# Kernel optimization log

Hardware: AMD Instinct MI355X
Metric: run time of the kernel (lower is better)

The kernel has to match this reference:

```python
import jax, jax.numpy as jnp
import numpy as np

B, D, W = 2048, 512, 512
DEPTH = 6
N_BINS = 2 ** DEPTH          # 64 leaves
N_NODES = 2 ** DEPTH - 1     # 63 inner nodes


def build_indices(depth: int) -> np.ndarray:
    """Root-to-leaf path index table into hstack([probs, 1-probs]).
    Index j selects probs[:, j]; index j + N selects 1 - probs[:, j]."""
    n = 2 ** depth - 1
    paths = []
    for b in range(2 ** depth):
        node, path = 0, []
        for level in range(depth):
            bit = (b >> (depth - 1 - level)) & 1
            path.append(node if bit == 0 else node + n)
            node = 2 * node + 1 + bit
        paths.append(path)
    return np.asarray(paths, dtype=np.int32)  # [2**depth, depth]


def setup_inputs() -> dict:
    key = jax.random.key(0)
    k1, k2, k3, k4 = jax.random.split(key, 4)
    x = jax.random.normal(k1, (B, D), dtype=jnp.float32)
    ray = jax.random.normal(k2, (1, D), dtype=jnp.float32)  # kaiming-normal init
    w_i = jnp.zeros((1, N_NODES), dtype=jnp.float32)
    b_i = jax.random.normal(k3, (1, N_NODES), dtype=jnp.float32)
    a_i = 5.0 * jnp.ones((1, N_NODES), dtype=jnp.float32)
    # kaiming-normal over fan_in = input_width
    inner_transforms = jax.random.normal(k4, (N_BINS, D, W), dtype=jnp.float32) * np.float32((2.0 / D) ** 0.5)
    idx = jnp.asarray(build_indices(DEPTH))  # [64, 6] int32
    return {"x": x, "ray": ray, "w_i": w_i, "b_i": b_i, "a_i": a_i,
            "inner_transforms": inner_transforms, "idx": idx}


def reference(x, ray, w_i, b_i, a_i, inner_transforms, idx):
    eps = 1e-8
    # angles: arccos(cosine_similarity(x, ray)) / pi  -> [B]
    xn = jnp.maximum(jnp.linalg.norm(x, axis=1), eps)
    rn = jnp.maximum(jnp.linalg.norm(ray, axis=1), eps)  # [1]
    cos = (x @ ray[0]) / (xn * rn)
    angles = jnp.arccos(cos) / jnp.pi  # [B]
    # per-node decision probabilities: [B, N_NODES]
    node_fns = (0.5 + jax.nn.sigmoid(w_i)) * angles[:, None] - jax.nn.sigmoid(b_i)
    decisions = jax.nn.sigmoid(node_fns * (1.0 + a_i))
    # tree-indexed gather + product over path -> soft bin distribution [B, N_BINS]
    stacked = jnp.concatenate([decisions, 1.0 - decisions], axis=1)  # [B, 2N]
    bins, depth = idx.shape
    gathered = stacked[:, idx.reshape(-1)].reshape(x.shape[0], bins, depth)
    distribution = jnp.prod(gathered, axis=2)  # [B, L]
    # per-bin linear transforms, weighted by the distribution
    inner = jnp.einsum('bi,liw->blw', x, inner_transforms)  # [B, L, W]
    return jnp.einsum('bl,blo->bo', distribution, inner)  # [B, W]
```

## Files before the change

### kernel.cpp

```cpp
#include <hip/hip_runtime.h>
#include <math.h>

typedef float  f32x4  __attribute__((ext_vector_type(4)));
typedef float  f32x2  __attribute__((ext_vector_type(2)));
typedef short  bf16x8 __attribute__((ext_vector_type(8)));
typedef unsigned short u16x8 __attribute__((ext_vector_type(8)));
typedef unsigned short u16x4 __attribute__((ext_vector_type(4)));

#define B_ROWS 2048
#define D_DIM  512
#define W_DIM  512
#define N_NODES 63
#define N_BINS  64
#define K_TOT   32768
#define DEPS    1e-12f

#define STR2(x) #x
#define WAITVM(n) asm volatile("s_waitcnt vmcnt(" STR2(n) ")" ::: "memory")

__device__ __forceinline__ unsigned short f2bf(float f) {
    union { float f; unsigned int u; } v; v.f = f;
    unsigned int u = v.u;
    return (unsigned short)((u + 0x7fffu + ((u >> 16) & 1u)) >> 16);
}

__device__ __forceinline__ float sigmoidf_(float z) {
    return 1.0f / (1.0f + expf(-z));
}

__device__ __forceinline__ void load_lds16(const void* g, void* l) {
    __builtin_amdgcn_global_load_lds(
        (const __attribute__((address_space(1))) unsigned int*)g,
        (__attribute__((address_space(3))) unsigned int*)l,
        16, 0, 0);
}

__global__ __launch_bounds__(256) void k_pre(
    const float* __restrict__ x, const float* __restrict__ ray,
    const float* __restrict__ w_i, const float* __restrict__ b_i,
    const float* __restrict__ a_i, const int* __restrict__ idx,
    const float* __restrict__ T,
    float* __restrict__ dist, unsigned short* __restrict__ xb,
    unsigned short* __restrict__ Tt)
{
    __shared__ float tile[64][65];
    const int bid = blockIdx.x;
    const int t   = threadIdx.x;

    if (bid < 4096) {
        const int i0 = (bid & 7) * 64;
        const int w0 = ((bid >> 3) & 7) * 64;
        const int l  = bid >> 6;

        const int w4 = (t & 15) * 4;
        const int ir = t >> 4;
        const float* src = T + ((size_t)(l * 512 + i0)) * 512 + w0;
#pragma unroll
        for (int p = 0; p < 4; ++p) {
            int i = ir + p * 16;
            f32x4 v = *(const f32x4*)(src + (size_t)i * 512 + w4);
            tile[i][w4 + 0] = v.x; tile[i][w4 + 1] = v.y;
            tile[i][w4 + 2] = v.z; tile[i][w4 + 3] = v.w;
        }
        __syncthreads();
#pragma unroll
        for (int rep = 0; rep < 2; ++rep) {
            int id = t + rep * 256;
            int w  = id >> 3;
            int c  = id & 7;
            u16x8 o;
#pragma unroll
            for (int j = 0; j < 8; ++j) o[j] = f2bf(tile[c * 8 + j][w]);
            *(u16x8*)(Tt + (size_t)(w0 + w) * K_TOT + l * 512 + i0 + c * 8) = o;
        }
        return;
    }

    const int pb   = bid - 4096;
    const int wid  = t >> 6;
    const int lane = t & 63;
    const int row  = pb * 4 + wid;
    const float* xr = x + (size_t)row * D_DIM;

    float dotv = 0.f, xx = 0.f, rr = 0.f;
#pragma unroll
    for (int j = 0; j < 2; ++j) {
        f32x4 xv = *(const f32x4*)(xr  + j * 256 + lane * 4);
        f32x4 rv = *(const f32x4*)(ray + j * 256 + lane * 4);
        dotv += xv.x * rv.x + xv.y * rv.y + xv.z * rv.z + xv.w * rv.w;
        xx   += xv.x * xv.x + xv.y * xv.y + xv.z * xv.z + xv.w * xv.w;
        rr   += rv.x * rv.x + rv.y * rv.y + rv.z * rv.z + rv.w * rv.w;
        u16x4 o;
        o[0] = f2bf(xv.x); o[1] = f2bf(xv.y); o[2] = f2bf(xv.z); o[3] = f2bf(xv.w);
        *(u16x4*)(xb + (size_t)row * D_DIM + j * 256 + lane * 4) = o;
    }
#pragma unroll
    for (int off = 1; off < 64; off <<= 1) {
        dotv += __shfl_xor(dotv, off, 64);
        xx   += __shfl_xor(xx,   off, 64);
        rr   += __shfl_xor(rr,   off, 64);
    }
    float xn = fmaxf(sqrtf(xx), 1e-8f);
    float rn = fmaxf(sqrtf(rr), 1e-8f);
    float cosv = dotv / (xn * rn);
    cosv = fminf(1.f, fmaxf(-1.f, cosv));
    float angle = acosf(cosv) * 0.31830988618379067f;

    float dec = 0.f;
    if (lane < N_NODES) {
        float sw = sigmoidf_(w_i[lane]);
        float sb = sigmoidf_(b_i[lane]);
        float nf = (0.5f + sw) * angle - sb;
        dec = sigmoidf_(nf * (1.0f + a_i[lane]));
    }

    float p = 1.f;
#pragma unroll
    for (int v = 0; v < 6; ++v) {
        int j = idx[lane * 6 + v];
        int node = (j < N_NODES) ? j : j - N_NODES;
        float d = __shfl(dec, node, 64);
        p *= (j < N_NODES) ? d : (1.0f - d);
    }
    dist[(size_t)row * N_BINS + lane] = p;
}

__global__ __launch_bounds__(512, 2) void k_gemm16(
    const unsigned short* __restrict__ xb, const unsigned short* __restrict__ Tt,
    const float* __restrict__ dist, float* __restrict__ part)
{
    __shared__ unsigned short As[2][256 * 64];
    __shared__ unsigned short Bs[2][256 * 64];
    __shared__ float distS[256 * 4];

    const int b    = blockIdx.x;
    const int xcd  = b & 7;
    const int g    = b >> 3;
    const int z    = xcd * 2 + (g & 1);
    const int tile = g >> 1;
    const int bm0  = (tile & 7) * 256;
    const int bn0  = (tile >> 3) * 256;
    const int l0   = z * 4;

    const int t    = threadIdx.x;
    const int lane = t & 63;
    const int wid  = t >> 6;
    const int wm   = wid >> 2;
    const int wn   = wid & 3;
    const int lq = lane >> 4, lr = lane & 15;

    const int srow = t >> 3;
    const int c    = t & 7;

    f32x4 acc[8][4];
#pragma unroll
    for (int a = 0; a < 8; ++a)
#pragma unroll
        for (int bb = 0; bb < 4; ++bb)
            acc[a][bb] = (f32x4){0.f, 0.f, 0.f, 0.f};

#define SGA(u_, slot_, g_)                                                    \
    {                                                                         \
        const int i0_  = ((u_) & 7) * 64;                                     \
        const int row_ = srow + (g_) * 64;                                    \
        const int cg_  = c ^ (row_ & 7);                                      \
        load_lds16(xb + (size_t)(bm0 + row_) * D_DIM + i0_ + cg_ * 8,         \
                   &As[slot_][row_ * 64 + c * 8]);                            \
    }
#define SGB(u_, slot_, g_)                                                    \
    {                                                                         \
        const int l_   = l0 + ((u_) >> 3);                                    \
        const int i0_  = ((u_) & 7) * 64;                                     \
        const int row_ = srow + (g_) * 64;                                    \
        const int cg_  = c ^ (row_ & 7);                                      \
        load_lds16(Tt + (size_t)(bn0 + row_) * K_TOT + (size_t)l_ * 512       \
                       + i0_ + cg_ * 8,                                       \
                   &Bs[slot_][row_ * 64 + c * 8]);                            \
    }

#define RD_A(dst, fmb)                                                        \
    _Pragma("unroll") for (int f = 0; f < 4; ++f)                             \
    _Pragma("unroll") for (int ks = 0; ks < 2; ++ks) {                        \
        int row = ((fmb) + f) * 32 + wm * 16 + lr;                            \
        dst[f][ks] = *(const bf16x8*)&As[rs][row * 64 +                       \
                       (((ks * 4 + lq) ^ (row & 7)) * 8)];                    \
    }
#define RD_B(dst, fnb)                                                        \
    _Pragma("unroll") for (int f = 0; f < 2; ++f)                             \
    _Pragma("unroll") for (int ks = 0; ks < 2; ++ks) {                        \
        int row = ((fnb) + f) * 64 + wn * 16 + lr;                            \
        dst[f][ks] = *(const bf16x8*)&Bs[rs][row * 64 +                       \
                       (((ks * 4 + lq) ^ (row & 7)) * 8)];                    \
    }
#define MM(fmb, afv, bfv, fnb)                                                \
    __builtin_amdgcn_s_setprio(1);                                            \
    _Pragma("unroll") for (int f = 0; f < 4; ++f)                             \
    _Pragma("unroll") for (int e = 0; e < 2; ++e)                             \
    _Pragma("unroll") for (int ks = 0; ks < 2; ++ks)                          \
        acc[(fmb) + f][(fnb) + e] = __builtin_amdgcn_mfma_f32_16x16x32_bf16(  \
            afv[f][ks], bfv[e][ks], acc[(fmb) + f][(fnb) + e], 0, 0, 0);      \
    __builtin_amdgcn_s_setprio(0);

#define LGKM0                                                                 \
    asm volatile("s_waitcnt lgkmcnt(0)" ::: "memory");                        \
    __builtin_amdgcn_sched_barrier(0);

#define TILE(u_, V0_, V1_, PF_)                                               \
  {                                                                           \
    const int rs = (u_) & 1, ss = rs ^ 1;                                     \
                                                       \
    RD_A(afr, 0) RD_B(bfr0, 0)                                                \
    if (PF_) { SGA((u_) + 1, ss, 0) SGA((u_) + 1, ss, 1) }                    \
    __builtin_amdgcn_s_barrier();                                             \
    LGKM0                                                                     \
    MM(0, afr, bfr0, 0)                                                       \
    WAITVM(V0_);                                                              \
    __builtin_amdgcn_s_barrier();                                             \
                                                       \
    RD_B(bfr1, 2)                                                             \
    if (PF_) { SGB((u_) + 1, ss, 0) SGB((u_) + 1, ss, 1) }                    \
    __builtin_amdgcn_s_barrier();                                             \
    LGKM0                                                                     \
    MM(0, afr, bfr1, 2)                                                       \
    WAITVM(V1_);                                                              \
    __builtin_amdgcn_s_barrier();                                             \
                                                       \
    RD_A(afr, 4)                                                              \
    if (PF_) { SGB((u_) + 1, ss, 2) SGB((u_) + 1, ss, 3) }                    \
    __builtin_amdgcn_s_barrier();                                             \
    LGKM0                                                                     \
    MM(4, afr, bfr0, 0)                                                       \
    __builtin_amdgcn_s_barrier();                                             \
                                                       \
    if (PF_) { SGA((u_) + 1, ss, 2) SGA((u_) + 1, ss, 3) }                    \
    __builtin_amdgcn_s_barrier();                                             \
    __builtin_amdgcn_sched_barrier(0);                                        \
    MM(4, afr, bfr1, 2)                                                       \
    WAITVM(4);                                                                \
    __builtin_amdgcn_s_barrier();                                             \
  }

    bf16x8 afr[4][2], bfr0[2][2], bfr1[2][2];

    if (t < 256)
        load_lds16(dist + (size_t)(bm0 + t) * N_BINS + l0, &distS[t * 4]);
    SGA(0, 0, 0) SGA(0, 0, 1)
    SGB(0, 0, 0) SGB(0, 0, 1)
    SGB(0, 0, 2) SGB(0, 0, 3)
    SGA(0, 0, 2) SGA(0, 0, 3)
    WAITVM(4);
    __builtin_amdgcn_s_barrier();

    for (int u = 0; u < 31; ++u) {
        if ((u & 7) == 0 && u > 0) {
            const int li = (u >> 3) - 1;
#pragma unroll
            for (int fm = 0; fm < 8; ++fm)
#pragma unroll
                for (int r = 0; r < 4; ++r) {
                    int ml = fm * 32 + wm * 16 + lq * 4 + r;
                    float dp = fmaxf(distS[ml * 4 + li],     DEPS);
                    float dn = fmaxf(distS[ml * 4 + li + 1], DEPS);
                    float ratio = dp * __builtin_amdgcn_rcpf(dn);
#pragma unroll
                    for (int fn = 0; fn < 4; ++fn)
                        acc[fm][fn][r] *= ratio;
                }
        }
        TILE(u, 4, 4, true)
    }
    TILE(31, 2, 0, false)

#undef TILE
#undef LGKM0
#undef MM
#undef RD_A
#undef RD_B
#undef SGA
#undef SGB

    float* Cp = part + (size_t)z * (B_ROWS * W_DIM);
#pragma unroll
    for (int fm = 0; fm < 8; ++fm)
#pragma unroll
        for (int r = 0; r < 4; ++r) {
            int ml = fm * 32 + wm * 16 + lq * 4 + r;
            float dv = fmaxf(distS[ml * 4 + 3], DEPS);
            int m = bm0 + ml;
#pragma unroll
            for (int fn = 0; fn < 4; ++fn) {
                int col = bn0 + fn * 64 + wn * 16 + lr;
                Cp[(size_t)m * W_DIM + col] = acc[fm][fn][r] * dv;
            }
        }
}

__global__ __launch_bounds__(512, 2) void k_gemm10(
    const unsigned short* __restrict__ xb, const unsigned short* __restrict__ Tt,
    const float* __restrict__ dist, float* __restrict__ part)
{
    __shared__ unsigned short As[3][256 * 64];
    __shared__ unsigned short Bs[3][128 * 64];

    const int b    = blockIdx.x;
    const int z    = b & 7;
    const int tile = b >> 3;
    const int bm0  = (tile & 7) * 256;
    const int bn0  = (tile >> 3) * 128;
    const int l0   = z * 8;

    const int t    = threadIdx.x;
    const int lane = t & 63;
    const int wid  = t >> 6;
    const int wm = wid >> 1, wn = wid & 1;
    const int lq = lane >> 4, lr = lane & 15;

    const int srow = t >> 3;
    const int c    = t & 7;

    f32x4 acc[4][4];
#pragma unroll
    for (int a = 0; a < 4; ++a)
#pragma unroll
        for (int bb = 0; bb < 4; ++bb)
            acc[a][bb] = (f32x4){0.f, 0.f, 0.f, 0.f};

#define STAGE_A(u_, slot_, g_)                                                \
    {                                                                         \
        const int i0_  = ((u_) & 7) * 64;                                     \
        const int row_ = srow + (g_) * 64;                                    \
        const int cg_  = c ^ (row_ & 7);                                      \
        load_lds16(xb + (size_t)(bm0 + row_) * D_DIM + i0_ + cg_ * 8,         \
                   &As[slot_][row_ * 64 + c * 8]);                            \
    }
#define STAGE_B(u_, slot_, g_)                                                \
    {                                                                         \
        const int l_   = l0 + ((u_) >> 3);                                    \
        const int i0_  = ((u_) & 7) * 64;                                     \
        const int row_ = srow + (g_) * 64;                                    \
        const int cg_  = c ^ (row_ & 7);                                      \
        load_lds16(Tt + (size_t)(bn0 + row_) * K_TOT + (size_t)l_ * 512       \
                       + i0_ + cg_ * 8,                                       \
                   &Bs[slot_][row_ * 64 + c * 8]);                            \
    }

    STAGE_A(0, 0, 0) STAGE_A(0, 0, 1) STAGE_A(0, 0, 2) STAGE_A(0, 0, 3)
    STAGE_B(0, 0, 0) STAGE_B(0, 0, 1)
    STAGE_A(1, 1, 0) STAGE_A(1, 1, 1) STAGE_A(1, 1, 2) STAGE_A(1, 1, 3)
    STAGE_B(1, 1, 0) STAGE_B(1, 1, 1)

    int rs = 0;
    for (int u = 0; u < 64; ++u) {
        if (u < 63) WAITVM(6);
        else        WAITVM(0);
        __builtin_amdgcn_s_barrier();

        if ((u & 7) == 0 && u > 0) {
            const int l = l0 + (u >> 3);
#pragma unroll
            for (int fm = 0; fm < 4; ++fm)
#pragma unroll
                for (int r = 0; r < 4; ++r) {
                    int m = bm0 + wm * 64 + fm * 16 + lq * 4 + r;
                    f32x2 dd = *(const f32x2*)(dist + (size_t)m * N_BINS + (l - 1));
                    float dp = fmaxf(dd.x, DEPS);
                    float dn = fmaxf(dd.y, DEPS);
                    float ratio = dp * __builtin_amdgcn_rcpf(dn);
#pragma unroll
                    for (int fn = 0; fn < 4; ++fn)
                        acc[fm][fn][r] *= ratio;
                }
        }

        const int ws_ = (rs == 0) ? 2 : rs - 1;
        const bool pf = (u + 2 < 64);

        {
            bf16x8 af[4], bfv[4];
#pragma unroll
            for (int fm = 0; fm < 4; ++fm) {
                int m = wm * 64 + fm * 16 + lr;
                af[fm] = *(const bf16x8*)&As[rs][m * 64 + ((lq ^ (m & 7)) * 8)];
            }
#pragma unroll
            for (int fn = 0; fn < 4; ++fn) {
                int n = wn * 64 + fn * 16 + lr;
                bfv[fn] = *(const bf16x8*)&Bs[rs][n * 64 + ((lq ^ (n & 7)) * 8)];
            }
            if (pf) { STAGE_A(u + 2, ws_, 0) STAGE_A(u + 2, ws_, 1) STAGE_A(u + 2, ws_, 2) }
            __builtin_amdgcn_s_setprio(1);
#pragma unroll
            for (int fm = 0; fm < 4; ++fm)
#pragma unroll
                for (int fn = 0; fn < 4; ++fn)
                    acc[fm][fn] = __builtin_amdgcn_mfma_f32_16x16x32_bf16(
                        af[fm], bfv[fn], acc[fm][fn], 0, 0, 0);
            __builtin_amdgcn_s_setprio(0);
        }
        __builtin_amdgcn_s_barrier();
        {
            bf16x8 af[4], bfv[4];
#pragma unroll
            for (int fm = 0; fm < 4; ++fm) {
                int m = wm * 64 + fm * 16 + lr;
                af[fm] = *(const bf16x8*)&As[rs][m * 64 + (((4 + lq) ^ (m & 7)) * 8)];
            }
#pragma unroll
            for (int fn = 0; fn < 4; ++fn) {
                int n = wn * 64 + fn * 16 + lr;
                bfv[fn] = *(const bf16x8*)&Bs[rs][n * 64 + (((4 + lq) ^ (n & 7)) * 8)];
            }
            if (pf) { STAGE_A(u + 2, ws_, 3) STAGE_B(u + 2, ws_, 0) STAGE_B(u + 2, ws_, 1) }
            __builtin_amdgcn_s_setprio(1);
#pragma unroll
            for (int fm = 0; fm < 4; ++fm)
#pragma unroll
                for (int fn = 0; fn < 4; ++fn)
                    acc[fm][fn] = __builtin_amdgcn_mfma_f32_16x16x32_bf16(
                        af[fm], bfv[fn], acc[fm][fn], 0, 0, 0);
            __builtin_amdgcn_s_setprio(0);
        }

        rs = (rs == 2) ? 0 : rs + 1;
    }
#undef STAGE_A
#undef STAGE_B

    float* Cp = part + (size_t)z * (B_ROWS * W_DIM);
#pragma unroll
    for (int fm = 0; fm < 4; ++fm)
#pragma unroll
        for (int r = 0; r < 4; ++r) {
            int m = bm0 + wm * 64 + fm * 16 + lq * 4 + r;
            float dl = fmaxf(dist[(size_t)m * N_BINS + (l0 + 7)], DEPS);
#pragma unroll
            for (int fn = 0; fn < 4; ++fn) {
                int col = bn0 + wn * 64 + fn * 16 + lr;
                Cp[(size_t)m * W_DIM + col] = acc[fm][fn][r] * dl;
            }
        }
}

__global__ __launch_bounds__(256) void k_reduce(
    const float* __restrict__ part, float* __restrict__ out, int nsplit)
{
    int i = (blockIdx.x * 256 + threadIdx.x) * 4;
    f32x4 s = *(const f32x4*)(part + i);
    for (int p = 1; p < nsplit; ++p)
        s += *(const f32x4*)(part + (size_t)p * (B_ROWS * W_DIM) + i);
    *(f32x4*)(out + i) = s;
}

__global__ __launch_bounds__(256, 2) void k_gemm_bt(
    const float* __restrict__ x, const float* __restrict__ dist,
    const unsigned short* __restrict__ Tt, float* __restrict__ part,
    int kchunk)
{
    __shared__ unsigned short As[128][72];
    __shared__ unsigned short Bs[128][64];

    const int bm0 = blockIdx.x * 128;
    const int bn0 = blockIdx.y * 128;
    const int kbase = blockIdx.z * kchunk;

    const int lane = threadIdx.x & 63;
    const int wid  = threadIdx.x >> 6;
    const int wm = wid >> 1, wn = wid & 1;
    const int lq = lane >> 4, lr = lane & 15;

    f32x4 acc[4][4];
#pragma unroll
    for (int a = 0; a < 4; ++a)
#pragma unroll
        for (int b = 0; b < 4; ++b)
            acc[a][b] = (f32x4){0.f, 0.f, 0.f, 0.f};

    const int iters = kchunk / 64;
    for (int it = 0; it < iters; ++it) {
        const int k0 = kbase + it * 64;
        const int l  = k0 >> 9;
        const int i0 = k0 & 511;
#pragma unroll
        for (int r2 = 0; r2 < 8; ++r2) {
            int id = threadIdx.x + r2 * 256;
            int m  = id >> 4;
            int kc = id & 15;
            float sc = dist[(size_t)(bm0 + m) * N_BINS + l];
            f32x4 v = *(const f32x4*)(x + (size_t)(bm0 + m) * D_DIM + i0 + kc * 4);
            v *= sc;
            unsigned int p0 = (unsigned int)f2bf(v.x) | ((unsigned int)f2bf(v.y) << 16);
            unsigned int p1 = (unsigned int)f2bf(v.z) | ((unsigned int)f2bf(v.w) << 16);
            unsigned int* dp = (unsigned int*)&As[m][kc * 4];
            dp[0] = p0; dp[1] = p1;
        }
#pragma unroll
        for (int r2 = 0; r2 < 4; ++r2) {
            int id = threadIdx.x + r2 * 256;
            int n  = id >> 3;
            int cc = id & 7;
            int cg = cc ^ (n & 7);
            const u16x8 v = *(const u16x8*)(Tt + (size_t)(bn0 + n) * K_TOT + k0 + cg * 8);
            *(u16x8*)&Bs[n][cc * 8] = v;
        }
        __syncthreads();
#pragma unroll
        for (int ks = 0; ks < 2; ++ks) {
            bf16x8 af[4], bfr[4];
#pragma unroll
            for (int fm = 0; fm < 4; ++fm)
                af[fm] = *(const bf16x8*)&As[wm * 64 + fm * 16 + lr][ks * 32 + lq * 8];
#pragma unroll
            for (int fn = 0; fn < 4; ++fn) {
                int nl = wn * 64 + fn * 16 + lr;
                int cs = (ks * 4 + lq) ^ (nl & 7);
                bfr[fn] = *(const bf16x8*)&Bs[nl][cs * 8];
            }
#pragma unroll
            for (int fm = 0; fm < 4; ++fm)
#pragma unroll
                for (int fn = 0; fn < 4; ++fn)
                    acc[fm][fn] = __builtin_amdgcn_mfma_f32_16x16x32_bf16(
                        af[fm], bfr[fn], acc[fm][fn], 0, 0, 0);
        }
        __syncthreads();
    }

    float* Cp = part + (size_t)blockIdx.z * (B_ROWS * W_DIM);
#pragma unroll
    for (int fm = 0; fm < 4; ++fm)
#pragma unroll
        for (int fn = 0; fn < 4; ++fn)
#pragma unroll
            for (int r = 0; r < 4; ++r) {
                int row = bm0 + wm * 64 + fm * 16 + lq * 4 + r;
                int col = bn0 + wn * 64 + fn * 16 + lr;
                Cp[(size_t)row * W_DIM + col] = acc[fm][fn][r];
            }
}

extern "C" void kernel_launch(void* const* d_in, const int* in_sizes, int n_in,
                              void* d_out, int out_size, void* d_ws, size_t ws_size,
                              hipStream_t stream) {
    const float* x   = (const float*)d_in[0];
    const float* ray = (const float*)d_in[1];
    const float* w_i = (const float*)d_in[2];
    const float* b_i = (const float*)d_in[3];
    const float* a_i = (const float*)d_in[4];
    const float* T   = (const float*)d_in[5];
    const int*   idx = (const int*)d_in[6];
    float* out = (float*)d_out;

    char* ws = (char*)d_ws;
    const size_t distBytes = (size_t)B_ROWS * N_BINS * 4;
    const size_t xbBytes   = (size_t)B_ROWS * D_DIM * 2;
    const size_t ttBytes   = (size_t)W_DIM * K_TOT * 2;
    const size_t partBytes = (size_t)B_ROWS * W_DIM * 4;

    float*          dist = (float*)ws;
    unsigned short* xb   = (unsigned short*)(ws + distBytes);
    unsigned short* Tt   = (unsigned short*)(ws + distBytes + xbBytes);
    float*          part = (float*)(ws + distBytes + xbBytes + ttBytes);

    const size_t base   = distBytes + xbBytes + ttBytes;
    const size_t need16 = base + 16 * partBytes;
    const size_t need8  = base + 8 * partBytes;

    if (ws_size >= need16) {
        k_pre<<<4096 + 512, 256, 0, stream>>>(x, ray, w_i, b_i, a_i, idx, T,
                                              dist, xb, Tt);
        k_gemm16<<<256, 512, 0, stream>>>(xb, Tt, dist, part);
        k_reduce<<<(B_ROWS * W_DIM) / (256 * 4), 256, 0, stream>>>(part, out, 16);
    } else if (ws_size >= need8) {
        k_pre<<<4096 + 512, 256, 0, stream>>>(x, ray, w_i, b_i, a_i, idx, T,
                                              dist, xb, Tt);
        k_gemm10<<<256, 512, 0, stream>>>(xb, Tt, dist, part);
        k_reduce<<<(B_ROWS * W_DIM) / (256 * 4), 256, 0, stream>>>(part, out, 8);
    } else if (ws_size >= base) {
        k_pre<<<4096 + 512, 256, 0, stream>>>(x, ray, w_i, b_i, a_i, idx, T,
                                              dist, xb, Tt);
        k_gemm_bt<<<dim3(16, 4, 1), 256, 0, stream>>>(x, dist, Tt, out, K_TOT);
    }
}
```

Before: 189.8 us.

## Restructure GEMM main loop to issue all LDS fragment reads up front

Replaces the TILE macro schedule with a loop that waits for all global-to-LDS prefetches at the top of each iteration, then issues every A and B fragment read from LDS before starting MFMAs. Partial lgkmcnt waits let the MFMAs start as soon as their operands arrive. Next-tile global prefetches are interleaved between MFMA groups. This adds an extra A fragment register set and a full vmcnt(0) wait per iteration, which may expose global latency and raise register pressure.

```diff
diff --git a/kernel.cpp b/kernel.cpp
--- a/kernel.cpp
+++ b/kernel.cpp
@@ -17,6 +17,7 @@
 
 #define STR2(x) #x
 #define WAITVM(n) asm volatile("s_waitcnt vmcnt(" STR2(n) ")" ::: "memory")
+#define WAITLG(n) asm volatile("s_waitcnt lgkmcnt(" STR2(n) ")" ::: "memory")
 
 __device__ __forceinline__ unsigned short f2bf(float f) {
     union { float f; unsigned int u; } v; v.f = f;
@@ -125,7 +126,7 @@
     dist[(size_t)row * N_BINS + lane] = p;
 }
 
-__global__ __launch_bounds__(512, 2) void k_gemm16(
+__global__ __launch_bounds__(512, 2) void k_gemm17(
     const unsigned short* __restrict__ xb, const unsigned short* __restrict__ Tt,
     const float* __restrict__ dist, float* __restrict__ part)
 {
@@ -201,57 +202,20 @@
             afv[f][ks], bfv[e][ks], acc[(fmb) + f][(fnb) + e], 0, 0, 0);      \
     __builtin_amdgcn_s_setprio(0);
 
-#define LGKM0                                                                 \
-    asm volatile("s_waitcnt lgkmcnt(0)" ::: "memory");                        \
-    __builtin_amdgcn_sched_barrier(0);
-
-#define TILE(u_, V0_, V1_, PF_)                                               \
-  {                                                                           \
-    const int rs = (u_) & 1, ss = rs ^ 1;                                     \
-                                                       \
-    RD_A(afr, 0) RD_B(bfr0, 0)                                                \
-    if (PF_) { SGA((u_) + 1, ss, 0) SGA((u_) + 1, ss, 1) }                    \
-    __builtin_amdgcn_s_barrier();                                             \
-    LGKM0                                                                     \
-    MM(0, afr, bfr0, 0)                                                       \
-    WAITVM(V0_);                                                              \
-    __builtin_amdgcn_s_barrier();                                             \
-                                                       \
-    RD_B(bfr1, 2)                                                             \
-    if (PF_) { SGB((u_) + 1, ss, 0) SGB((u_) + 1, ss, 1) }                    \
-    __builtin_amdgcn_s_barrier();                                             \
-    LGKM0                                                                     \
-    MM(0, afr, bfr1, 2)                                                       \
-    WAITVM(V1_);                                                              \
-    __builtin_amdgcn_s_barrier();                                             \
-                                                       \
-    RD_A(afr, 4)                                                              \
-    if (PF_) { SGB((u_) + 1, ss, 2) SGB((u_) + 1, ss, 3) }                    \
-    __builtin_amdgcn_s_barrier();                                             \
-    LGKM0                                                                     \
-    MM(4, afr, bfr0, 0)                                                       \
-    __builtin_amdgcn_s_barrier();                                             \
-                                                       \
-    if (PF_) { SGA((u_) + 1, ss, 2) SGA((u_) + 1, ss, 3) }                    \
-    __builtin_amdgcn_s_barrier();                                             \
-    __builtin_amdgcn_sched_barrier(0);                                        \
-    MM(4, afr, bfr1, 2)                                                       \
-    WAITVM(4);                                                                \
-    __builtin_amdgcn_s_barrier();                                             \
-  }
-
-    bf16x8 afr[4][2], bfr0[2][2], bfr1[2][2];
+    bf16x8 afr[4][2], afr2[4][2], bfr0[2][2], bfr1[2][2];
 
     if (t < 256)
         load_lds16(dist + (size_t)(bm0 + t) * N_BINS + l0, &distS[t * 4]);
-    SGA(0, 0, 0) SGA(0, 0, 1)
-    SGB(0, 0, 0) SGB(0, 0, 1)
-    SGB(0, 0, 2) SGB(0, 0, 3)
-    SGA(0, 0, 2) SGA(0, 0, 3)
-    WAITVM(4);
-    __builtin_amdgcn_s_barrier();
-
-    for (int u = 0; u < 31; ++u) {
+    SGA(0, 0, 0) SGA(0, 0, 1) SGA(0, 0, 2) SGA(0, 0, 3)
+    SGB(0, 0, 0) SGB(0, 0, 1) SGB(0, 0, 2) SGB(0, 0, 3)
+
+    for (int u = 0; u < 32; ++u) {
+        const int rs = u & 1, ss = rs ^ 1;
+        const bool pf = (u + 1 < 32);
+
+        WAITVM(0);
+        __builtin_amdgcn_s_barrier();
+
         if ((u & 7) == 0 && u > 0) {
             const int li = (u >> 3) - 1;
 #pragma unroll
@@ -266,13 +230,37 @@
                     for (int fn = 0; fn < 4; ++fn)
                         acc[fm][fn][r] *= ratio;
                 }
-        }
-        TILE(u, 4, 4, true)
-    }
-    TILE(31, 2, 0, false)
-
-#undef TILE
-#undef LGKM0
+            WAITLG(0);
+            __builtin_amdgcn_sched_barrier(0);
+        }
+
+        RD_A(afr, 0) RD_B(bfr0, 0)
+        __builtin_amdgcn_sched_barrier(0);
+        RD_B(bfr1, 2)
+        __builtin_amdgcn_sched_barrier(0);
+        RD_A(afr2, 4)
+        __builtin_amdgcn_sched_barrier(0);
+        if (pf) { SGA(u + 1, ss, 0) SGA(u + 1, ss, 1)
+                  SGB(u + 1, ss, 0) SGB(u + 1, ss, 1) }
+        __builtin_amdgcn_s_barrier();
+        WAITLG(12); __builtin_amdgcn_sched_barrier(0);
+        MM(0, afr, bfr0, 0)
+        __builtin_amdgcn_s_barrier();
+
+        if (pf) { SGB(u + 1, ss, 2) SGB(u + 1, ss, 3)
+                  SGA(u + 1, ss, 2) SGA(u + 1, ss, 3) }
+        __builtin_amdgcn_s_barrier();
+        WAITLG(8); __builtin_amdgcn_sched_barrier(0);
+        MM(0, afr, bfr1, 2)
+        __builtin_amdgcn_s_barrier();
+
+        WAITLG(0); __builtin_amdgcn_sched_barrier(0);
+        MM(4, afr2, bfr0, 0)
+        __builtin_amdgcn_s_barrier();
+
+        MM(4, afr2, bfr1, 2)
+    }
+
 #undef MM
 #undef RD_A
 #undef RD_B
@@ -568,7 +556,7 @@
     if (ws_size >= need16) {
         k_pre<<<4096 + 512, 256, 0, stream>>>(x, ray, w_i, b_i, a_i, idx, T,
                                               dist, xb, Tt);
-        k_gemm16<<<256, 512, 0, stream>>>(xb, Tt, dist, part);
+        k_gemm17<<<256, 512, 0, stream>>>(xb, Tt, dist, part);
         k_reduce<<<(B_ROWS * W_DIM) / (256 * 4), 256, 0, stream>>>(part, out, 16);
     } else if (ws_size >= need8) {
         k_pre<<<4096 + 512, 256, 0, stream>>>(x, ray, w_i, b_i, a_i, idx, T,
```

Result: no change. 192.6 us (+1.4%).
